# Optimization experiments

Hardware: AMD Instinct MI355X
Metric: run time of the kernel (lower is better)

The kernel has to match this reference:

```python
import math
import jax, jax.numpy as jnp
import numpy as np

D_MODEL = 1024
NUM_HEADS = 16
HEAD_DIM = D_MODEL // NUM_HEADS
THETA = 10000.0
MAX_SEQ_LEN = 2048
BATCH = 4
SEQ = 2048


def _rope_tables():
    # angles[i, j] = i / theta**(2j/d_k), shapes [max_seq_len, head_dim//2]
    i = jnp.arange(MAX_SEQ_LEN, dtype=jnp.float32)
    k = jnp.arange(0, HEAD_DIM, 2, dtype=jnp.float32) / HEAD_DIM
    angles = i[:, None] * (1.0 / (THETA ** k))[None, :]
    return jnp.cos(angles), jnp.sin(angles)


def _apply_rope(x, token_positions, cos_tab, sin_tab):
    # x: [b, h, s, d_k]; token_positions: [s]
    b, h, s, dk = x.shape
    xr = x.reshape(b, h, s, dk // 2, 2)
    x0, x1 = xr[..., 0], xr[..., 1]
    cos_pos = cos_tab[token_positions]  # [s, dk//2]
    sin_pos = sin_tab[token_positions]
    x0_rot = x0 * cos_pos - x1 * sin_pos
    x1_rot = x0 * sin_pos + x1 * cos_pos
    return jnp.stack([x0_rot, x1_rot], axis=-1).reshape(x.shape)


def setup_inputs() -> dict:
    key = jax.random.key(0)
    k1, k2, k3 = jax.random.split(key, 3)
    std_qkv = math.sqrt(2.0 / (D_MODEL + 3 * D_MODEL))
    std_o = math.sqrt(2.0 / (D_MODEL + D_MODEL))
    return {
        "x": jax.random.normal(k1, (BATCH, SEQ, D_MODEL), dtype=jnp.float32),
        "token_positions": jnp.arange(SEQ, dtype=jnp.int64) if jax.config.jax_enable_x64 else jnp.arange(SEQ, dtype=jnp.int32),
        "qkv_w": jax.random.normal(k2, (3 * D_MODEL, D_MODEL), dtype=jnp.float32) * std_qkv,
        "o_w": jax.random.normal(k3, (D_MODEL, D_MODEL), dtype=jnp.float32) * std_o,
    }


def reference(x, token_positions, qkv_w, o_w):
    b, s, _ = x.shape
    cos_tab, sin_tab = _rope_tables()
    # fused QKV projection: [b, s, 3*d_model]
    qkv = jnp.einsum('bsd,ed->bse', x, qkv_w)
    qkv = qkv.reshape(b, s, 3, NUM_HEADS, HEAD_DIM)
    q = jnp.transpose(qkv[:, :, 0], (0, 2, 1, 3))  # [b, h, s, hd]
    k = jnp.transpose(qkv[:, :, 1], (0, 2, 1, 3))
    v = jnp.transpose(qkv[:, :, 2], (0, 2, 1, 3))
    q = _apply_rope(q, token_positions, cos_tab, sin_tab)
    k = _apply_rope(k, token_positions, cos_tab, sin_tab)
    # causal mask and eager softmax attention (full [b,h,s,s] scores)
    scores = jnp.einsum('bhnk,bhmk->bhnm', q, k) / math.sqrt(HEAD_DIM)
    causal = jnp.tril(jnp.ones((s, s), dtype=bool))
    scores = jnp.where(causal, scores, -jnp.inf)
    attn = jax.nn.softmax(scores, axis=-1)
    ctx = jnp.einsum('bhnm,bhmv->bhnv', attn, v)
    ctx = jnp.transpose(ctx, (0, 2, 1, 3)).reshape(b, s, D_MODEL)
    return jnp.einsum('bsd,ed->bse', ctx, o_w)
```

## Files before the change

### kernel.cpp

```cpp
#include <hip/hip_runtime.h>


#define DM   1024
#define NH   16
#define HD   64
#define SEQL 2048
#define BATCH 4
#define QKV_ELEMS 8388608

using short8 = __attribute__((ext_vector_type(8))) short;
using f32x4  = __attribute__((ext_vector_type(4))) float;
typedef unsigned short u16;

#define WAIT_VM(n) __builtin_amdgcn_s_waitcnt(0x0F70 | (n))
#define WAIT_LGKM0() __builtin_amdgcn_s_waitcnt(0xC07F)
#define BARRIER()  __builtin_amdgcn_s_barrier()

__device__ __forceinline__ unsigned cvtpk(float lo, float hi) {
    unsigned r;
    asm("v_cvt_pk_bf16_f32 %0, %1, %2" : "=v"(r) : "v"(lo), "v"(hi));
    return r;
}
__device__ __forceinline__ u16 f2bf1(float x) {
    unsigned r;
    asm("v_cvt_pk_bf16_f32 %0, %1, %1" : "=v"(r) : "v"(x));
    return (u16)r;
}
__device__ __forceinline__ float fexp2(float x) {
#if __has_builtin(__builtin_amdgcn_exp2f)
    return __builtin_amdgcn_exp2f(x);
#else
    return __expf(x * 0.6931471805599453f);
#endif
}

__device__ __forceinline__ void load16(const void* g, void* l) {
    __builtin_amdgcn_global_load_lds(
        (__attribute__((address_space(1))) unsigned int*)(unsigned long long)g,
        (__attribute__((address_space(3))) unsigned int*)(unsigned int)(unsigned long long)l,
        16, 0, 0);
}

__global__ __launch_bounds__(256) void prep(const float* __restrict__ x, u16* __restrict__ xb,
                                            const float* __restrict__ qw, u16* __restrict__ wb,
                                            const float* __restrict__ ow, u16* __restrict__ owb,
                                            float* __restrict__ cost, float* __restrict__ sint) {
    int bx = blockIdx.x;
    if (bx < 12288) {
        const float* in; u16* out; int i;
        if (bx < 8192)       { in = x;  out = xb;  i = bx * 256 + threadIdx.x; }
        else if (bx < 11264) { in = qw; out = wb;  i = (bx - 8192) * 256 + threadIdx.x; }
        else                 { in = ow; out = owb; i = (bx - 11264) * 256 + threadIdx.x; }
        float4 v = ((const float4*)in)[i];
        uint2 o;
        o.x = cvtpk(v.x, v.y);
        o.y = cvtpk(v.z, v.w);
        ((uint2*)out)[i] = o;
    } else {
        int t = (bx - 12288) * 256 + threadIdx.x;
        int j = t & 31, pos = t >> 5;
        float freq = exp2f((float)j * (-2.0f / 64.0f) * 13.287712379549449f);
        float ang = (float)pos * freq;
        cost[t] = cosf(ang);
        sint[t] = sinf(ang);
    }
}

__device__ __forceinline__ void gemm128_core(const u16* __restrict__ A,
                                             const u16* __restrict__ B,
                                             int K, int m0, int n0,
                                             u16* As, u16* Bs, f32x4 acc[4][4]) {
    int tid = threadIdx.x, w = tid >> 6, l = tid & 63;
    int l15 = l & 15, l4 = l >> 4;
    int wm = w >> 1, wn = w & 1;
    int r0 = 32 * w + (l >> 2);
    int gblk = ((l & 3) ^ ((l >> 4) & 3)) * 8;
    const u16* gA0 = A + (size_t)(m0 + r0) * K + gblk;
    const u16* gA1 = gA0 + (size_t)16 * K;
    const u16* gB0 = B + (size_t)(n0 + r0) * K + gblk;
    const u16* gB1 = gB0 + (size_t)16 * K;
    char* ldsA = (char*)As + 2048 * w;
    char* ldsB = (char*)Bs + 2048 * w;
    int fo = ((l4 ^ (l15 >> 2)) & 3) * 16;
    f32x4 z = {0.f, 0.f, 0.f, 0.f};
#pragma unroll
    for (int i = 0; i < 4; ++i)
#pragma unroll
        for (int j = 0; j < 4; ++j) acc[i][j] = z;
    int nk = K >> 5;
#pragma unroll
    for (int t = 0; t < 2; ++t) {
        int ko = t << 5, nb = t * 8192;
        load16(gA0 + ko, ldsA + nb); load16(gA1 + ko, ldsA + nb + 1024);
        load16(gB0 + ko, ldsB + nb); load16(gB1 + ko, ldsB + nb + 1024);
    }
    int buf = 0;
    for (int kt = 0; kt < nk; ++kt) {
        if (kt < nk - 1) WAIT_VM(4); else WAIT_VM(0);
        BARRIER();
        if (kt + 2 < nk) {
            int ko = (kt + 2) << 5;
            int nb = 8192 * ((buf + 2) % 3);
            load16(gA0 + ko, ldsA + nb); load16(gA1 + ko, ldsA + nb + 1024);
            load16(gB0 + ko, ldsB + nb); load16(gB1 + ko, ldsB + nb + 1024);
        }
        const char* bA = (const char*)As + 8192 * buf;
        const char* bB = (const char*)Bs + 8192 * buf;
        short8 a[4], b[4];
#pragma unroll
        for (int i = 0; i < 4; ++i)
            a[i] = *(const short8*)(bA + (64 * wm + 16 * i + l15) * 64 + fo);
#pragma unroll
        for (int j = 0; j < 4; ++j)
            b[j] = *(const short8*)(bB + (64 * wn + 16 * j + l15) * 64 + fo);
#pragma unroll
        for (int i = 0; i < 4; ++i)
#pragma unroll
            for (int j = 0; j < 4; ++j)
                acc[i][j] = __builtin_amdgcn_mfma_f32_16x16x32_bf16(a[i], b[j], acc[i][j], 0, 0, 0);
        buf = (buf + 1) % 3;
    }
}

__global__ __launch_bounds__(512, 2) void gemm_qkv(const u16* __restrict__ xb,
                                                   const u16* __restrict__ wb,
                                                   u16* __restrict__ qkv,
                                                   u16* __restrict__ vt,
                                                   const int* __restrict__ pos_ids,
                                                   const float* __restrict__ cost,
                                                   const float* __restrict__ sint) {
    __shared__ __align__(16) u16 As[3 * 256 * 32];
    __shared__ __align__(16) u16 Bs[3 * 256 * 32];
    int tid = threadIdx.x, w = tid >> 6, l = tid & 63;
    int l15 = l & 15, l4 = l >> 4;
    int wr = w >> 2, wc = w & 3;

    int bid = blockIdx.y * 12 + blockIdx.x;
    int swz = (bid & 7) * 48 + (bid >> 3);
    int nI = swz % 12, mI = swz / 12;
    int m0 = mI * 256, n0 = nI * 256;

    int schunk = ((l & 3) ^ ((l >> 3) & 3)) * 8;
    const u16* gA = xb + (size_t)(m0 + 32 * w + (l >> 2)) * DM + schunk;
    const u16* gB = wb + (size_t)(n0 + 32 * w + (l >> 2)) * DM + schunk;
    char* ldsA = (char*)As + 2048 * w;
    char* ldsB = (char*)Bs + 2048 * w;

    int roff = (l4 ^ ((l15 >> 1) & 3)) * 16;
    int aoff = (128 * wr + l15) * 64 + roff;
    int boff = (64 * wc + l15) * 64 + roff;

    f32x4 acc[8][4];
    f32x4 z = {0.f, 0.f, 0.f, 0.f};
#pragma unroll
    for (int i = 0; i < 8; ++i)
#pragma unroll
        for (int j = 0; j < 4; ++j) acc[i][j] = z;

#pragma unroll
    for (int t = 0; t < 2; ++t) {
        load16(gA + t * 32,           ldsA + t * 16384);
        load16(gA + t * 32 + 16 * DM, ldsA + t * 16384 + 1024);
        load16(gB + t * 32,           ldsB + t * 16384);
        load16(gB + t * 32 + 16 * DM, ldsB + t * 16384 + 1024);
    }
    WAIT_VM(4);
    BARRIER();

    int buf = 0;
    for (int kt = 0; kt < 32; ++kt) {
        const char* bA = (const char*)As + 16384 * buf;
        const char* bB = (const char*)Bs + 16384 * buf;
        int nb = buf + 2; if (nb >= 3) nb -= 3;
        short8 a[4], b[4];
#pragma unroll
        for (int i = 0; i < 4; ++i) a[i] = *(const short8*)(bA + aoff + 1024 * i);
#pragma unroll
        for (int j = 0; j < 4; ++j) b[j] = *(const short8*)(bB + boff + 1024 * j);
        if (kt + 2 < 32) {
            load16(gA + (kt + 2) * 32,           ldsA + nb * 16384);
            load16(gA + (kt + 2) * 32 + 16 * DM, ldsA + nb * 16384 + 1024);
        }
        BARRIER();
        WAIT_LGKM0();
        __builtin_amdgcn_s_setprio(1);
#pragma unroll
        for (int i = 0; i < 4; ++i)
#pragma unroll
            for (int j = 0; j < 4; ++j)
                acc[i][j] = __builtin_amdgcn_mfma_f32_16x16x32_bf16(a[i], b[j], acc[i][j], 0, 0, 0);
        __builtin_amdgcn_s_setprio(0);
        BARRIER();
        short8 a2[4];
#pragma unroll
        for (int i = 0; i < 4; ++i) a2[i] = *(const short8*)(bA + aoff + 1024 * (i + 4));
        if (kt + 2 < 32) {
            load16(gB + (kt + 2) * 32,           ldsB + nb * 16384);
            load16(gB + (kt + 2) * 32 + 16 * DM, ldsB + nb * 16384 + 1024);
        }
        BARRIER();
        WAIT_LGKM0();
        __builtin_amdgcn_s_setprio(1);
#pragma unroll
        for (int i = 0; i < 4; ++i)
#pragma unroll
            for (int j = 0; j < 4; ++j)
                acc[i + 4][j] = __builtin_amdgcn_mfma_f32_16x16x32_bf16(a2[i], b[j], acc[i + 4][j], 0, 0, 0);
        __builtin_amdgcn_s_setprio(0);
        if (kt + 2 < 32) WAIT_VM(4); else WAIT_VM(0);
        BARRIER();
        buf = (kt + 1) % 3;
    }

    if (nI >= 8) {
#pragma unroll
        for (int j = 0; j < 4; ++j) {
            int nv = (n0 - 2048) + 64 * wc + 16 * j + l15;
            int h = nv >> 6, d = nv & 63;
#pragma unroll
            for (int i = 0; i < 8; ++i) {
                int sb = m0 + 128 * wr + 16 * i + 4 * l4;
                int bb = sb >> 11, s = sb & 2047;
                uint2 pk;
                pk.x = cvtpk(acc[i][j][0], acc[i][j][1]);
                pk.y = cvtpk(acc[i][j][2], acc[i][j][3]);
                *(uint2*)&vt[((size_t)(bb * 16 + h) * HD + d) * SEQL + s] = pk;
            }
        }
    } else {
        float sc = (nI < 4) ? 0.18033688011112042f : 1.0f;
        u16* base = qkv + (size_t)(nI >> 2) * QKV_ELEMS;
        int h = ((n0 & 1023) >> 6) + wc;
#pragma unroll
        for (int i = 0; i < 8; ++i) {
#pragma unroll
            for (int r = 0; r < 4; ++r) {
                int m = m0 + 128 * wr + 16 * i + 4 * l4 + r;
                int bb = m >> 11, s = m & 2047;
                int pos = pos_ids[s];
                const float* cr = cost + pos * 32;
                const float* sr = sint + pos * 32;
                u16* orow = base + ((size_t)(bb * 16 + h) * SEQL + s) * HD;
#pragma unroll
                for (int j = 0; j < 4; ++j) {
                    int d = 16 * j + l15, d2 = d >> 1;
                    float c  = cr[d2];
                    float sn = sr[d2];
                    float v  = acc[i][j][r];
                    float vp = __shfl_xor(v, 1);
                    float o  = (d & 1) ? (vp * sn + v * c) : (v * c - vp * sn);
                    orow[d] = f2bf1(o * sc);
                }
            }
        }
    }
}

__global__ __launch_bounds__(256) void gemm_out(const u16* __restrict__ ctx,
                                                const u16* __restrict__ owb,
                                                float* __restrict__ out) {
    __shared__ __align__(16) u16 As[3 * 128 * 32], Bs[3 * 128 * 32];
    f32x4 acc[4][4];
    int m0 = blockIdx.y * 128, n0 = blockIdx.x * 128;
    gemm128_core(ctx, owb, DM, m0, n0, As, Bs, acc);
    int l = threadIdx.x & 63, w = threadIdx.x >> 6;
    int l15 = l & 15, l4 = l >> 4;
    int wm = w >> 1, wn = w & 1;
#pragma unroll
    for (int i = 0; i < 4; ++i) {
        int mb = m0 + 64 * wm + 16 * i + 4 * l4;
#pragma unroll
        for (int j = 0; j < 4; ++j) {
            int n = n0 + 64 * wn + 16 * j + l15;
#pragma unroll
            for (int r = 0; r < 4; ++r)
                out[(size_t)(mb + r) * DM + n] = acc[i][j][r];
        }
    }
}

__device__ __forceinline__ void flash_pass(int qt, const u16* __restrict__ Qb,
                                           const u16* __restrict__ Kb,
                                           const u16* __restrict__ Vb,
                                           u16* __restrict__ ctx, int bh,
                                           u16* KsB, u16* VsB, u16* PsB) {
    int tid = threadIdx.x, w = tid >> 6, l = tid & 63;
    int l15 = l & 15, l4 = l >> 4;
    int q0 = qt * 256;
    int swz = l15 & 7;
    int b0 = (l4 ^ swz) * 16;

    short8 aq[2][2];
#pragma unroll
    for (int g = 0; g < 2; ++g) {
        const u16* qr = Qb + (size_t)(q0 + 128 * g + 16 * w + l15) * HD;
        aq[g][0] = *(const short8*)&qr[l4 * 8];
        aq[g][1] = *(const short8*)&qr[32 + l4 * 8];
    }
    int srow = l >> 3;
    int sblk = ((l & 7) ^ srow) * 8;
    const u16* gK = Kb + (size_t)(8 * w + srow) * HD + sblk;
    const u16* gV = Vb + (size_t)(8 * w + srow) * SEQL + sblk;
    char* ldsK = (char*)KsB + 1024 * w;
    char* ldsV = (char*)VsB + 1024 * w;
    char* prow0 = (char*)PsB + 2048 * w + l15 * 128;
    char* prow1 = prow0 + 16384;

    f32x4 z = {0.f, 0.f, 0.f, 0.f};
    f32x4 O[2][4] = {{z, z, z, z}, {z, z, z, z}};
    float lsum[2] = {0.f, 0.f};
    int nk = 4 * qt + 4;
    int d0 = 4 * qt + (w >> 2);
    int rowlim = 16 * (w & 3) + l15;

    BARRIER();
#pragma unroll
    for (int t = 0; t < 2; ++t) {
        load16(gK + (size_t)(t * 64) * HD, ldsK + t * 8192);
        load16(gV + t * 64,                ldsV + t * 8192);
    }
    int buf = 0;
    for (int it = 0; it < nk; ++it) {
        if (it < nk - 1) WAIT_VM(2); else WAIT_VM(0);
        BARRIER();
        if (it + 2 < nk) {
            int k0n = (it + 2) * 64;
            int nb = 8192 * ((buf + 2) % 3);
            load16(gK + (size_t)k0n * HD, ldsK + nb);
            load16(gV + k0n,              ldsV + nb);
        }
        if (it <= d0 + 2) {
            const char* bK = (const char*)KsB + 8192 * buf;
            const char* bV = (const char*)VsB + 8192 * buf;
            bool g0act = (it <= d0);
            short8 kf[4][2];
#pragma unroll
            for (int c = 0; c < 4; ++c) {
                const char* kr = bK + (16 * c + l15) * 128;
                kf[c][0] = *(const short8*)(kr + b0);
                kf[c][1] = *(const short8*)(kr + (b0 ^ 64));
            }
            if (g0act) {
                f32x4 S[4];
                __builtin_amdgcn_s_setprio(1);
#pragma unroll
                for (int c = 0; c < 4; ++c) {
                    S[c] = __builtin_amdgcn_mfma_f32_16x16x32_bf16(kf[c][0], aq[0][0], z, 0, 0, 0);
                    S[c] = __builtin_amdgcn_mfma_f32_16x16x32_bf16(kf[c][1], aq[0][1], S[c], 0, 0, 0);
                }
                __builtin_amdgcn_s_setprio(0);
                if (it == d0) {
#pragma unroll
                    for (int c = 0; c < 4; ++c)
#pragma unroll
                        for (int r = 0; r < 4; ++r)
                            if (16 * c + 4 * l4 + r > rowlim) S[c][r] = -3e38f;
                }
                float ls = 0.f;
#pragma unroll
                for (int c = 0; c < 4; ++c) {
                    float cs = 0.f;
#pragma unroll
                    for (int r = 0; r < 4; ++r) {
                        float p = fexp2(S[c][r]);
                        S[c][r] = p;
                        cs += p;
                    }
                    ls += cs;
                    uint2 pk;
                    pk.x = cvtpk(S[c][0], S[c][1]);
                    pk.y = cvtpk(S[c][2], S[c][3]);
                    *(uint2*)(prow0 + ((((2 * c + (l4 >> 1)) ^ swz) << 4) | ((l4 & 1) << 3))) = pk;
                }
                lsum[0] += ls;
            }
            {
                f32x4 S[4];
                __builtin_amdgcn_s_setprio(1);
#pragma unroll
                for (int c = 0; c < 4; ++c) {
                    S[c] = __builtin_amdgcn_mfma_f32_16x16x32_bf16(kf[c][0], aq[1][0], z, 0, 0, 0);
                    S[c] = __builtin_amdgcn_mfma_f32_16x16x32_bf16(kf[c][1], aq[1][1], S[c], 0, 0, 0);
                }
                __builtin_amdgcn_s_setprio(0);
                if (it == d0 + 2) {
#pragma unroll
                    for (int c = 0; c < 4; ++c)
#pragma unroll
                        for (int r = 0; r < 4; ++r)
                            if (16 * c + 4 * l4 + r > rowlim) S[c][r] = -3e38f;
                }
                float ls = 0.f;
#pragma unroll
                for (int c = 0; c < 4; ++c) {
                    float cs = 0.f;
#pragma unroll
                    for (int r = 0; r < 4; ++r) {
                        float p = fexp2(S[c][r]);
                        S[c][r] = p;
                        cs += p;
                    }
                    ls += cs;
                    uint2 pk;
                    pk.x = cvtpk(S[c][0], S[c][1]);
                    pk.y = cvtpk(S[c][2], S[c][3]);
                    *(uint2*)(prow1 + ((((2 * c + (l4 >> 1)) ^ swz) << 4) | ((l4 & 1) << 3))) = pk;
                }
                lsum[1] += ls;
            }
            short8 vf[4][2];
#pragma unroll
            for (int c = 0; c < 4; ++c) {
                const char* vr = bV + (16 * c + l15) * 128;
                vf[c][0] = *(const short8*)(vr + b0);
                vf[c][1] = *(const short8*)(vr + (b0 ^ 64));
            }
            if (g0act) {
                short8 ap0 = *(const short8*)(prow0 + b0);
                short8 ap1 = *(const short8*)(prow0 + (b0 ^ 64));
                __builtin_amdgcn_s_setprio(1);
#pragma unroll
                for (int nt = 0; nt < 4; ++nt) {
                    O[0][nt] = __builtin_amdgcn_mfma_f32_16x16x32_bf16(ap0, vf[nt][0], O[0][nt], 0, 0, 0);
                    O[0][nt] = __builtin_amdgcn_mfma_f32_16x16x32_bf16(ap1, vf[nt][1], O[0][nt], 0, 0, 0);
                }
                __builtin_amdgcn_s_setprio(0);
            }
            {
                short8 bp0 = *(const short8*)(prow1 + b0);
                short8 bp1 = *(const short8*)(prow1 + (b0 ^ 64));
                __builtin_amdgcn_s_setprio(1);
#pragma unroll
                for (int nt = 0; nt < 4; ++nt) {
                    O[1][nt] = __builtin_amdgcn_mfma_f32_16x16x32_bf16(bp0, vf[nt][0], O[1][nt], 0, 0, 0);
                    O[1][nt] = __builtin_amdgcn_mfma_f32_16x16x32_bf16(bp1, vf[nt][1], O[1][nt], 0, 0, 0);
                }
                __builtin_amdgcn_s_setprio(0);
            }
        }
        buf = (buf + 1) % 3;
    }
    int b = bh >> 4, h = bh & 15;
#pragma unroll
    for (int g = 0; g < 2; ++g) {
        float ls = lsum[g];
        ls += __shfl_xor(ls, 16);
        ls += __shfl_xor(ls, 32);
        float linv[4];
#pragma unroll
        for (int r = 0; r < 4; ++r) linv[r] = 1.0f / __shfl(ls, 20 * l4 + r);
#pragma unroll
        for (int nt = 0; nt < 4; ++nt) {
            int d = 16 * nt + l15;
#pragma unroll
            for (int r = 0; r < 4; ++r) {
                int s = q0 + 128 * g + 16 * w + 4 * l4 + r;
                ctx[((size_t)(b * SEQL + s)) * DM + h * 64 + d] = f2bf1(O[g][nt][r] * linv[r]);
            }
        }
    }
}

__global__ __launch_bounds__(512, 2) void flash_attn(const u16* __restrict__ Q,
                                                     const u16* __restrict__ K,
                                                     const u16* __restrict__ Vt,
                                                     u16* __restrict__ ctx) {
    __shared__ __align__(16) u16 Ks[3][64 * 64];
    __shared__ __align__(16) u16 Vs[3][64 * 64];
    __shared__ __align__(16) u16 Ps[2][8][16 * 64];
    int bh = blockIdx.y, pair = blockIdx.x;
    const u16* Qb = Q + (size_t)bh * SEQL * HD;
    const u16* Kb = K + (size_t)bh * SEQL * HD;
    const u16* Vb = Vt + (size_t)bh * HD * SEQL;
    flash_pass(7 - pair, Qb, Kb, Vb, ctx, bh, &Ks[0][0], &Vs[0][0], &Ps[0][0][0]);
    flash_pass(pair,     Qb, Kb, Vb, ctx, bh, &Ks[0][0], &Vs[0][0], &Ps[0][0][0]);
}

extern "C" void kernel_launch(void* const* d_in, const int* in_sizes, int n_in,
                              void* d_out, int out_size, void* d_ws, size_t ws_size,
                              hipStream_t stream) {
    const float* x     = (const float*)d_in[0];
    const int*   pos   = (const int*)d_in[1];
    const float* qkv_w = (const float*)d_in[2];
    const float* o_w   = (const float*)d_in[3];
    float* out = (float*)d_out;

    char* ws = (char*)d_ws;
    u16*   xb   = (u16*)(ws);
    u16*   wb   = (u16*)(ws + 16777216);
    u16*   owb  = (u16*)(ws + 23068672);
    float* cost = (float*)(ws + 25165824);
    float* sint = (float*)(ws + 25427968);
    u16*   qkv  = (u16*)(ws + 25690112);
    u16*   vt   = (u16*)(ws + 76021760);
    u16*   ctx  = xb;

    prep<<<12544, 256, 0, stream>>>(x, xb, qkv_w, wb, o_w, owb, cost, sint);
    gemm_qkv<<<dim3(12, 32), 512, 0, stream>>>(xb, wb, qkv, vt, pos, cost, sint);
    flash_attn<<<dim3(4, 64), 512, 0, stream>>>(qkv, qkv + QKV_ELEMS, vt, ctx);
    gemm_out<<<dim3(8, 64), 256, 0, stream>>>(ctx, owb, out);
}
```

Before: 237.4 us.

## Rewrite output GEMM as 256x128 tiled, phase-pipelined kernel; interleave RoPE cos/sin table

```diff
diff --git a/kernel.cpp b/kernel.cpp
--- a/kernel.cpp
+++ b/kernel.cpp
@@ -44,7 +44,7 @@
 __global__ __launch_bounds__(256) void prep(const float* __restrict__ x, u16* __restrict__ xb,
                                             const float* __restrict__ qw, u16* __restrict__ wb,
                                             const float* __restrict__ ow, u16* __restrict__ owb,
-                                            float* __restrict__ cost, float* __restrict__ sint) {
+                                            float2* __restrict__ cst) {
     int bx = blockIdx.x;
     if (bx < 12288) {
         const float* in; u16* out; int i;
@@ -61,64 +61,8 @@
         int j = t & 31, pos = t >> 5;
         float freq = exp2f((float)j * (-2.0f / 64.0f) * 13.287712379549449f);
         float ang = (float)pos * freq;
-        cost[t] = cosf(ang);
-        sint[t] = sinf(ang);
-    }
-}
-
-__device__ __forceinline__ void gemm128_core(const u16* __restrict__ A,
-                                             const u16* __restrict__ B,
-                                             int K, int m0, int n0,
-                                             u16* As, u16* Bs, f32x4 acc[4][4]) {
-    int tid = threadIdx.x, w = tid >> 6, l = tid & 63;
-    int l15 = l & 15, l4 = l >> 4;
-    int wm = w >> 1, wn = w & 1;
-    int r0 = 32 * w + (l >> 2);
-    int gblk = ((l & 3) ^ ((l >> 4) & 3)) * 8;
-    const u16* gA0 = A + (size_t)(m0 + r0) * K + gblk;
-    const u16* gA1 = gA0 + (size_t)16 * K;
-    const u16* gB0 = B + (size_t)(n0 + r0) * K + gblk;
-    const u16* gB1 = gB0 + (size_t)16 * K;
-    char* ldsA = (char*)As + 2048 * w;
-    char* ldsB = (char*)Bs + 2048 * w;
-    int fo = ((l4 ^ (l15 >> 2)) & 3) * 16;
-    f32x4 z = {0.f, 0.f, 0.f, 0.f};
-#pragma unroll
-    for (int i = 0; i < 4; ++i)
-#pragma unroll
-        for (int j = 0; j < 4; ++j) acc[i][j] = z;
-    int nk = K >> 5;
-#pragma unroll
-    for (int t = 0; t < 2; ++t) {
-        int ko = t << 5, nb = t * 8192;
-        load16(gA0 + ko, ldsA + nb); load16(gA1 + ko, ldsA + nb + 1024);
-        load16(gB0 + ko, ldsB + nb); load16(gB1 + ko, ldsB + nb + 1024);
-    }
-    int buf = 0;
-    for (int kt = 0; kt < nk; ++kt) {
-        if (kt < nk - 1) WAIT_VM(4); else WAIT_VM(0);
-        BARRIER();
-        if (kt + 2 < nk) {
-            int ko = (kt + 2) << 5;
-            int nb = 8192 * ((buf + 2) % 3);
-            load16(gA0 + ko, ldsA + nb); load16(gA1 + ko, ldsA + nb + 1024);
-            load16(gB0 + ko, ldsB + nb); load16(gB1 + ko, ldsB + nb + 1024);
-        }
-        const char* bA = (const char*)As + 8192 * buf;
-        const char* bB = (const char*)Bs + 8192 * buf;
-        short8 a[4], b[4];
-#pragma unroll
-        for (int i = 0; i < 4; ++i)
-            a[i] = *(const short8*)(bA + (64 * wm + 16 * i + l15) * 64 + fo);
-#pragma unroll
-        for (int j = 0; j < 4; ++j)
-            b[j] = *(const short8*)(bB + (64 * wn + 16 * j + l15) * 64 + fo);
-#pragma unroll
-        for (int i = 0; i < 4; ++i)
-#pragma unroll
-            for (int j = 0; j < 4; ++j)
-                acc[i][j] = __builtin_amdgcn_mfma_f32_16x16x32_bf16(a[i], b[j], acc[i][j], 0, 0, 0);
-        buf = (buf + 1) % 3;
+        float2 cs; cs.x = cosf(ang); cs.y = sinf(ang);
+        cst[t] = cs;
     }
 }
 
@@ -127,8 +71,7 @@
                                                    u16* __restrict__ qkv,
                                                    u16* __restrict__ vt,
                                                    const int* __restrict__ pos_ids,
-                                                   const float* __restrict__ cost,
-                                                   const float* __restrict__ sint) {
+                                                   const float2* __restrict__ cst) {
     __shared__ __align__(16) u16 As[3 * 256 * 32];
     __shared__ __align__(16) u16 Bs[3 * 256 * 32];
     int tid = threadIdx.x, w = tid >> 6, l = tid & 63;
@@ -231,6 +174,7 @@
         float sc = (nI < 4) ? 0.18033688011112042f : 1.0f;
         u16* base = qkv + (size_t)(nI >> 2) * QKV_ELEMS;
         int h = ((n0 & 1023) >> 6) + wc;
+        int d2b = l15 >> 1;
 #pragma unroll
         for (int i = 0; i < 8; ++i) {
 #pragma unroll
@@ -238,14 +182,16 @@
                 int m = m0 + 128 * wr + 16 * i + 4 * l4 + r;
                 int bb = m >> 11, s = m & 2047;
                 int pos = pos_ids[s];
-                const float* cr = cost + pos * 32;
-                const float* sr = sint + pos * 32;
+                const float2* ct = cst + pos * 32;
+                float2 tt[4];
+                tt[0] = ct[d2b];      tt[1] = ct[8 + d2b];
+                tt[2] = ct[16 + d2b]; tt[3] = ct[24 + d2b];
                 u16* orow = base + ((size_t)(bb * 16 + h) * SEQL + s) * HD;
 #pragma unroll
                 for (int j = 0; j < 4; ++j) {
-                    int d = 16 * j + l15, d2 = d >> 1;
-                    float c  = cr[d2];
-                    float sn = sr[d2];
+                    int d = 16 * j + l15;
+                    float c  = tt[j].x;
+                    float sn = tt[j].y;
                     float v  = acc[i][j][r];
                     float vp = __shfl_xor(v, 1);
                     float o  = (d & 1) ? (vp * sn + v * c) : (v * c - vp * sn);
@@ -256,22 +202,96 @@
     }
 }
 
-__global__ __launch_bounds__(256) void gemm_out(const u16* __restrict__ ctx,
-                                                const u16* __restrict__ owb,
-                                                float* __restrict__ out) {
-    __shared__ __align__(16) u16 As[3 * 128 * 32], Bs[3 * 128 * 32];
-    f32x4 acc[4][4];
-    int m0 = blockIdx.y * 128, n0 = blockIdx.x * 128;
-    gemm128_core(ctx, owb, DM, m0, n0, As, Bs, acc);
-    int l = threadIdx.x & 63, w = threadIdx.x >> 6;
+__global__ __launch_bounds__(512, 2) void gemm_out(const u16* __restrict__ ctx,
+                                                   const u16* __restrict__ owb,
+                                                   float* __restrict__ out) {
+    __shared__ __align__(16) u16 As[3 * 256 * 32];
+    __shared__ __align__(16) u16 Bs[3 * 128 * 32];
+    int tid = threadIdx.x, w = tid >> 6, l = tid & 63;
     int l15 = l & 15, l4 = l >> 4;
-    int wm = w >> 1, wn = w & 1;
-#pragma unroll
-    for (int i = 0; i < 4; ++i) {
-        int mb = m0 + 64 * wm + 16 * i + 4 * l4;
-#pragma unroll
-        for (int j = 0; j < 4; ++j) {
-            int n = n0 + 64 * wn + 16 * j + l15;
+    int wr = w >> 2, wc = w & 3;
+
+    int bid = blockIdx.y * 8 + blockIdx.x;
+    int swz = (bid & 7) * 32 + (bid >> 3);
+    int mI = swz >> 3, nI = swz & 7;
+    int m0 = mI * 256, n0 = nI * 128;
+
+    int schunk = ((l & 3) ^ ((l >> 3) & 3)) * 8;
+    const u16* gA = ctx + (size_t)(m0 + 32 * w + (l >> 2)) * DM + schunk;
+    const u16* gB = owb + (size_t)(n0 + 16 * w + (l >> 2)) * DM + schunk;
+    char* ldsA = (char*)As + 2048 * w;
+    char* ldsB = (char*)Bs + 1024 * w;
+
+    int roff = (l4 ^ ((l15 >> 1) & 3)) * 16;
+    int aoff = (128 * wr + l15) * 64 + roff;
+    int boff = (32 * wc + l15) * 64 + roff;
+
+    f32x4 acc[8][2];
+    f32x4 z = {0.f, 0.f, 0.f, 0.f};
+#pragma unroll
+    for (int i = 0; i < 8; ++i)
+#pragma unroll
+        for (int j = 0; j < 2; ++j) acc[i][j] = z;
+
+#pragma unroll
+    for (int t = 0; t < 2; ++t) {
+        load16(gA + t * 32,           ldsA + t * 16384);
+        load16(gA + t * 32 + 16 * DM, ldsA + t * 16384 + 1024);
+        load16(gB + t * 32,           ldsB + t * 8192);
+    }
+    WAIT_VM(3);
+    BARRIER();
+
+    int buf = 0;
+    for (int kt = 0; kt < 32; ++kt) {
+        const char* bA = (const char*)As + 16384 * buf;
+        const char* bB = (const char*)Bs + 8192 * buf;
+        int nb = buf + 2; if (nb >= 3) nb -= 3;
+        short8 a[4], b[2];
+#pragma unroll
+        for (int i = 0; i < 4; ++i) a[i] = *(const short8*)(bA + aoff + 1024 * i);
+#pragma unroll
+        for (int j = 0; j < 2; ++j) b[j] = *(const short8*)(bB + boff + 1024 * j);
+        if (kt + 2 < 32) {
+            load16(gA + (kt + 2) * 32,           ldsA + nb * 16384);
+            load16(gA + (kt + 2) * 32 + 16 * DM, ldsA + nb * 16384 + 1024);
+        }
+        BARRIER();
+        WAIT_LGKM0();
+        __builtin_amdgcn_s_setprio(1);
+#pragma unroll
+        for (int i = 0; i < 4; ++i)
+#pragma unroll
+            for (int j = 0; j < 2; ++j)
+                acc[i][j] = __builtin_amdgcn_mfma_f32_16x16x32_bf16(a[i], b[j], acc[i][j], 0, 0, 0);
+        __builtin_amdgcn_s_setprio(0);
+        BARRIER();
+        short8 a2[4];
+#pragma unroll
+        for (int i = 0; i < 4; ++i) a2[i] = *(const short8*)(bA + aoff + 1024 * (i + 4));
+        if (kt + 2 < 32) {
+            load16(gB + (kt + 2) * 32, ldsB + nb * 8192);
+        }
+        BARRIER();
+        WAIT_LGKM0();
+        __builtin_amdgcn_s_setprio(1);
+#pragma unroll
+        for (int i = 0; i < 4; ++i)
+#pragma unroll
+            for (int j = 0; j < 2; ++j)
+                acc[i + 4][j] = __builtin_amdgcn_mfma_f32_16x16x32_bf16(a2[i], b[j], acc[i + 4][j], 0, 0, 0);
+        __builtin_amdgcn_s_setprio(0);
+        if (kt + 2 < 32) WAIT_VM(3); else WAIT_VM(0);
+        BARRIER();
+        buf = (kt + 1) % 3;
+    }
+
+#pragma unroll
+    for (int i = 0; i < 8; ++i) {
+        int mb = m0 + 128 * wr + 16 * i + 4 * l4;
+#pragma unroll
+        for (int j = 0; j < 2; ++j) {
+            int n = n0 + 32 * wc + 16 * j + l15;
 #pragma unroll
             for (int r = 0; r < 4; ++r)
                 out[(size_t)(mb + r) * DM + n] = acc[i][j][r];
@@ -486,17 +506,16 @@
     float* out = (float*)d_out;
 
     char* ws = (char*)d_ws;
-    u16*   xb   = (u16*)(ws);
-    u16*   wb   = (u16*)(ws + 16777216);
-    u16*   owb  = (u16*)(ws + 23068672);
-    float* cost = (float*)(ws + 25165824);
-    float* sint = (float*)(ws + 25427968);
-    u16*   qkv  = (u16*)(ws + 25690112);
-    u16*   vt   = (u16*)(ws + 76021760);
-    u16*   ctx  = xb;
-
-    prep<<<12544, 256, 0, stream>>>(x, xb, qkv_w, wb, o_w, owb, cost, sint);
-    gemm_qkv<<<dim3(12, 32), 512, 0, stream>>>(xb, wb, qkv, vt, pos, cost, sint);
+    u16*    xb  = (u16*)(ws);
+    u16*    wb  = (u16*)(ws + 16777216);
+    u16*    owb = (u16*)(ws + 23068672);
+    float2* cst = (float2*)(ws + 25165824);
+    u16*    qkv = (u16*)(ws + 25690112);
+    u16*    vt  = (u16*)(ws + 76021760);
+    u16*    ctx = xb;
+
+    prep<<<12544, 256, 0, stream>>>(x, xb, qkv_w, wb, o_w, owb, cst);
+    gemm_qkv<<<dim3(12, 32), 512, 0, stream>>>(xb, wb, qkv, vt, pos, cst);
     flash_attn<<<dim3(4, 64), 512, 0, stream>>>(qkv, qkv + QKV_ELEMS, vt, ctx);
-    gemm_out<<<dim3(8, 64), 256, 0, stream>>>(ctx, owb, out);
-}
+    gemm_out<<<dim3(8, 32), 512, 0, stream>>>(ctx, owb, out);
+}
```

Result: slower. 243.5 us (+2.6%).
